# Kernel optimization log

Measured on AMD Instinct MI355X. Metric: run time of the kernel, lower is better.

Reference implementation:

```python
import jax, jax.numpy as jnp
import numpy as np
import math

D_MODEL = 1024
D_HIDDEN = 64
H = 16
B = 2
N = 2048


def softmax_one(x, axis=-1):
    # exp(x - max) / (1 + sum(exp(x - max))) -- matches the torch code exactly
    m = jnp.max(x, axis=axis, keepdims=True)
    e = jnp.exp(x - m)
    return e / (1.0 + jnp.sum(e, axis=axis, keepdims=True))


def setup_inputs() -> dict:
    key = jax.random.key(0)
    ks = jax.random.split(key, 8)
    queries = jax.random.normal(ks[0], (B, N, D_MODEL), dtype=jnp.float32)
    keys = jax.random.normal(ks[1], (B, N, D_MODEL), dtype=jnp.float32)
    values = jax.random.normal(ks[2], (B, N, D_MODEL), dtype=jnp.float32)
    std = 0.02
    Wq = std * jax.random.normal(ks[3], (H * D_HIDDEN, D_MODEL), dtype=jnp.float32)
    Wk = std * jax.random.normal(ks[4], (H * D_HIDDEN, D_MODEL), dtype=jnp.float32)
    Wv = std * jax.random.normal(ks[5], (H * D_HIDDEN, D_MODEL), dtype=jnp.float32)
    Wo = std * jax.random.normal(ks[6], (D_MODEL, H * D_HIDDEN), dtype=jnp.float32)
    bq = jnp.zeros((H * D_HIDDEN,), jnp.float32)
    bk = jnp.zeros((H * D_HIDDEN,), jnp.float32)
    bv = jnp.zeros((H * D_HIDDEN,), jnp.float32)
    bo = jnp.zeros((D_MODEL,), jnp.float32)
    return {"queries": queries, "keys": keys, "values": values,
            "Wq": Wq, "bq": bq, "Wk": Wk, "bk": bk,
            "Wv": Wv, "bv": bv, "Wo": Wo, "bo": bo}


def reference(queries, keys, values, Wq, bq, Wk, bk, Wv, bv, Wo, bo):
    b_s, nq, _ = queries.shape
    nk = keys.shape[1]
    # projections: (b, n, h*dh) -> (b, h, n, dh)
    q = (queries @ Wq.T + bq).reshape(b_s, nq, H, D_HIDDEN).transpose(0, 2, 1, 3)
    k = (keys @ Wk.T + bk).reshape(b_s, nk, H, D_HIDDEN).transpose(0, 2, 1, 3)
    v = (values @ Wv.T + bv).reshape(b_s, nk, H, D_HIDDEN).transpose(0, 2, 1, 3)
    scale = 1.0 / math.sqrt(D_HIDDEN)
    scores = jnp.einsum('bhqd,bhkd->bhqk', q, k) * scale  # (b, h, nq, nk)
    attn = softmax_one(scores, axis=-1)  # dropout disabled (eval)
    out = jnp.einsum('bhqk,bhkd->bhqd', attn, v)  # (b, h, nq, dh)
    out = out.transpose(0, 2, 1, 3).reshape(b_s, nq, H * D_HIDDEN)
    out = out @ Wo.T + bo
    present = jnp.stack((k, v))  # (2, b, h, nk, dh)
    return (out, present)
```

## Files before the change

kernel.cpp:

```cpp
#include <hip/hip_runtime.h>
#include <math.h>

#define D_MODEL 1024
#define DH 64
#define NH 16
#define BS 2
#define SEQ 2048
#define MTOT (BS*SEQ)

typedef _Float16 f16x8 __attribute__((ext_vector_type(8)));
typedef _Float16 f16x4 __attribute__((ext_vector_type(4)));
typedef float f32x4 __attribute__((ext_vector_type(4)));
typedef unsigned int u32;

__device__ __forceinline__ void load_lds16(const void* g, void* l) {
    __builtin_amdgcn_global_load_lds(
        (const __attribute__((address_space(1))) u32*)g,
        (__attribute__((address_space(3))) u32*)l, 16, 0, 0);
}

__global__ __launch_bounds__(256) void convert_all_kernel(
    const float* __restrict__ s0, const float* __restrict__ s1, const float* __restrict__ s2,
    const float* __restrict__ s3, const float* __restrict__ s4, const float* __restrict__ s5,
    const float* __restrict__ s6,
    _Float16* __restrict__ d0, _Float16* __restrict__ d1, _Float16* __restrict__ d2,
    _Float16* __restrict__ d3, _Float16* __restrict__ d4, _Float16* __restrict__ d5,
    _Float16* __restrict__ d6, int nX, int nW)
{
    int y = blockIdx.y;
    const float* s; _Float16* d; int n;
    switch (y) {
        case 0: s = s0; d = d0; n = nX; break;
        case 1: s = s1; d = d1; n = nX; break;
        case 2: s = s2; d = d2; n = nX; break;
        case 3: s = s3; d = d3; n = nW; break;
        case 4: s = s4; d = d4; n = nW; break;
        case 5: s = s5; d = d5; n = nW; break;
        default: s = s6; d = d6; n = nW; break;
    }
    int i = (blockIdx.x * 256 + threadIdx.x) * 8;
    if (i < n) {
        float4 a = *(const float4*)(s + i);
        float4 b = *(const float4*)(s + i + 4);
        f16x8 o;
        o[0] = (_Float16)a.x; o[1] = (_Float16)a.y; o[2] = (_Float16)a.z; o[3] = (_Float16)a.w;
        o[4] = (_Float16)b.x; o[5] = (_Float16)b.y; o[6] = (_Float16)b.z; o[7] = (_Float16)b.w;
        *(f16x8*)(d + i) = o;
    }
}

__global__ __launch_bounds__(256) void qkv_proj_kernel(
    const _Float16* __restrict__ Xq, const _Float16* __restrict__ Xk, const _Float16* __restrict__ Xv,
    const _Float16* __restrict__ Wq, const _Float16* __restrict__ Wk, const _Float16* __restrict__ Wv,
    const float* __restrict__ bq, const float* __restrict__ bk, const float* __restrict__ bv,
    _Float16* __restrict__ qh, _Float16* __restrict__ kh,
    float* __restrict__ outp)
{
    __shared__ __align__(16) _Float16 ldsA[128][64];
    __shared__ __align__(16) _Float16 ldsB[128][64];

    const int jb = blockIdx.x >> 5;
    const int ib = blockIdx.x & 31;
    const int id = jb >> 3;
    const int col0 = (jb & 7) << 7;
    const int row0 = ib << 7;

    const _Float16* X  = (id == 0) ? Xq : (id == 1) ? Xk : Xv;
    const _Float16* W  = (id == 0) ? Wq : (id == 1) ? Wk : Wv;
    const float* bias  = (id == 0) ? bq : (id == 1) ? bk : bv;

    const int tid = threadIdx.x;
    const int w = tid >> 6, lane = tid & 63;
    const int quad = lane >> 4, l16 = lane & 15;
    const int wm = (w >> 1) << 6, wn = (w & 1) << 6;

    const int r_loc = lane >> 3;
    const int sg = ((lane & 7) ^ r_loc) << 3;

    const f32x4 zero = {0.f, 0.f, 0.f, 0.f};
    f32x4 acc[4][4];
#pragma unroll
    for (int i = 0; i < 4; i++)
#pragma unroll
        for (int j = 0; j < 4; j++) acc[i][j] = zero;

    for (int k0 = 0; k0 < D_MODEL; k0 += 64) {
        __syncthreads();
#pragma unroll
        for (int i = 0; i < 4; i++) {
            int r = i * 32 + w * 8 + r_loc;
            load_lds16(X + (size_t)(row0 + r) * D_MODEL + k0 + sg, &ldsA[i * 32 + w * 8][0]);
            load_lds16(W + (size_t)(col0 + r) * D_MODEL + k0 + sg, &ldsB[i * 32 + w * 8][0]);
        }
        __syncthreads();
#pragma unroll
        for (int kk = 0; kk < 2; kk++) {
            f16x8 af[4], bfr[4];
#pragma unroll
            for (int mi = 0; mi < 4; mi++)
                af[mi]  = *(const f16x8*)&ldsA[wm + mi*16 + l16][(((kk<<2) + quad) ^ (l16 & 7)) << 3];
#pragma unroll
            for (int ni = 0; ni < 4; ni++)
                bfr[ni] = *(const f16x8*)&ldsB[wn + ni*16 + l16][(((kk<<2) + quad) ^ (l16 & 7)) << 3];
#pragma unroll
            for (int mi = 0; mi < 4; mi++)
#pragma unroll
                for (int ni = 0; ni < 4; ni++)
                    acc[mi][ni] = __builtin_amdgcn_mfma_f32_16x16x32_f16(af[mi], bfr[ni], acc[mi][ni], 0, 0, 0);
        }
    }

    const size_t OUT0 = (size_t)MTOT * D_MODEL;
    const size_t PRES = (size_t)BS * NH * SEQ * DH;
#pragma unroll
    for (int ni = 0; ni < 4; ni++) {
        int gn = col0 + wn + ni * 16 + l16;
        float bias_v = bias[gn];
        int h = gn >> 6, d = gn & 63;
#pragma unroll
        for (int mi = 0; mi < 4; mi++) {
#pragma unroll
            for (int r = 0; r < 4; r++) {
                int gm = row0 + wm + mi * 16 + quad * 4 + r;
                float val = acc[mi][ni][r] + bias_v;
                int b = gm >> 11, n = gm & 2047;
                size_t bh = (size_t)(b * NH + h);
                size_t idx = (bh * SEQ + n) * DH + d;
                if (id == 0) {
                    qh[idx] = (_Float16)val;
                } else if (id == 1) {
                    outp[OUT0 + idx] = val;
                    kh[idx] = (_Float16)val;
                } else {
                    outp[OUT0 + PRES + idx] = val;
                }
            }
        }
    }
}

__global__ __launch_bounds__(256) void vtrans_kernel(
    const float* __restrict__ p1, _Float16* __restrict__ vt)
{
    const int bh = blockIdx.x >> 6, nt = blockIdx.x & 63;
    const int tid = threadIdx.x;
    const int d = tid & 63, n8 = tid >> 6;
    const int n0 = nt * 32 + n8 * 8;
    const float* src = p1 + ((size_t)bh * SEQ + n0) * DH + d;
    f16x8 o;
#pragma unroll
    for (int i = 0; i < 8; i++) o[i] = (_Float16)src[(size_t)i * DH];
    *(f16x8*)(vt + ((size_t)bh * DH + d) * SEQ + n0) = o;
}

__global__ __launch_bounds__(512) void attn_kernel(
    const _Float16* __restrict__ qh, const _Float16* __restrict__ kh,
    const _Float16* __restrict__ vt, _Float16* __restrict__ aout)
{
    __shared__ __align__(16) _Float16 Kt[2][64][76];
    __shared__ __align__(16) _Float16 Vt[2][64][76];

    const int bh = blockIdx.x & 31;
    const int qt = blockIdx.x >> 5;
    const int b = bh >> 4, h = bh & 15;
    const int tid = threadIdx.x;
    const int w = tid >> 6, lane = tid & 63;
    const int quad = lane >> 4, l16 = lane & 15;
    const int qr0 = qt * 128 + w * 16;

    const _Float16* Qb = qh + (size_t)bh * SEQ * DH;
    const _Float16* Kb = kh + (size_t)bh * SEQ * DH;
    const _Float16* Vb = vt + (size_t)bh * DH * SEQ;

    const float QSCALE = 0.125f * 1.44269504f;
    f16x8 aq[2];
#pragma unroll
    for (int ks = 0; ks < 2; ks++) {
        f16x8 t = *(const f16x8*)(Qb + (size_t)(qr0 + l16) * DH + ks * 32 + quad * 8);
#pragma unroll
        for (int j = 0; j < 8; j++) t[j] = (_Float16)((float)t[j] * QSCALE);
        aq[ks] = t;
    }

    const int sr = tid >> 3, sc = (tid & 7) << 3;

    *(f16x8*)&Kt[0][sr][sc] = *(const f16x8*)(Kb + (size_t)sr * DH + sc);
    *(f16x8*)&Vt[0][sr][sc] = *(const f16x8*)(Vb + (size_t)sr * SEQ + sc);
    __syncthreads();

    float m2 = -INFINITY, lsum = 0.f;
    const f32x4 zero = {0.f, 0.f, 0.f, 0.f};
    f32x4 accO[4];
#pragma unroll
    for (int db = 0; db < 4; db++) accO[db] = zero;

    for (int t = 0; t < SEQ / 64; t++) {
        const int cur = t & 1;
        const int kc = t * 64;

        f16x8 kr, vr;
        if (t + 1 < SEQ / 64) {
            kr = *(const f16x8*)(Kb + (size_t)(kc + 64 + sr) * DH + sc);
            vr = *(const f16x8*)(Vb + (size_t)sr * SEQ + kc + 64 + sc);
        }

        f32x4 sT[4];
#pragma unroll
        for (int nb = 0; nb < 4; nb++) sT[nb] = zero;
#pragma unroll
        for (int ks = 0; ks < 2; ks++)
#pragma unroll
            for (int nb = 0; nb < 4; nb++) {
                f16x8 kf = *(const f16x8*)&Kt[cur][nb*16 + l16][ks*32 + quad*8];
                sT[nb] = __builtin_amdgcn_mfma_f32_16x16x32_f16(kf, aq[ks], sT[nb], 0, 0, 0);
            }

        f16x4 pf[4];
#pragma unroll
        for (int nb = 0; nb < 4; nb++)
#pragma unroll
            for (int r = 0; r < 4; r++) {
                float s = sT[nb][r];
                m2 = fmaxf(m2, s);
                float e = __builtin_amdgcn_exp2f(s);
                lsum += e;
                pf[nb][r] = (_Float16)e;
            }

#pragma unroll
        for (int db = 0; db < 4; db++)
#pragma unroll
            for (int nb = 0; nb < 4; nb++) {
                f16x4 vf = *(const f16x4*)&Vt[cur][db*16 + l16][nb*16 + quad*4];
                accO[db] = __builtin_amdgcn_mfma_f32_16x16x16f16(vf, pf[nb], accO[db], 0, 0, 0);
            }

        if (t + 1 < SEQ / 64) {
            *(f16x8*)&Kt[cur ^ 1][sr][sc] = kr;
            *(f16x8*)&Vt[cur ^ 1][sr][sc] = vr;
        }
        __syncthreads();
    }

    m2 = fmaxf(m2, __shfl_xor(m2, 16));
    m2 = fmaxf(m2, __shfl_xor(m2, 32));
    lsum += __shfl_xor(lsum, 16);
    lsum += __shfl_xor(lsum, 32);

    const float inv = 1.f / (__builtin_amdgcn_exp2f(m2) + lsum);
    const int q = qr0 + l16;
    _Float16* orow = aout + ((size_t)b * SEQ + q) * D_MODEL + h * DH + quad * 4;
#pragma unroll
    for (int db = 0; db < 4; db++) {
        f16x4 o;
#pragma unroll
        for (int r = 0; r < 4; r++) o[r] = (_Float16)(accO[db][r] * inv);
        *(f16x4*)(orow + db * 16) = o;
    }
}

__global__ __launch_bounds__(256) void out_proj_kernel(
    const _Float16* __restrict__ aout, const _Float16* __restrict__ Wo,
    const float* __restrict__ bo, float* __restrict__ outp)
{
    __shared__ __align__(16) _Float16 ldsA[64][64];
    __shared__ __align__(16) _Float16 ldsB[128][64];

    const int jb = blockIdx.x >> 6;
    const int ib = blockIdx.x & 63;
    const int col0 = jb << 7, row0 = ib << 6;
    const int tid = threadIdx.x;
    const int w = tid >> 6, lane = tid & 63;
    const int quad = lane >> 4, l16 = lane & 15;
    const int wm = (w >> 1) << 5, wn = (w & 1) << 6;

    const int r_loc = lane >> 3;
    const int sg = ((lane & 7) ^ r_loc) << 3;

    const f32x4 zero = {0.f, 0.f, 0.f, 0.f};
    f32x4 acc[2][4];
#pragma unroll
    for (int i = 0; i < 2; i++)
#pragma unroll
        for (int j = 0; j < 4; j++) acc[i][j] = zero;

    for (int k0 = 0; k0 < D_MODEL; k0 += 64) {
        __syncthreads();
#pragma unroll
        for (int i = 0; i < 2; i++) {
            int r = i * 32 + w * 8 + r_loc;
            load_lds16(aout + (size_t)(row0 + r) * D_MODEL + k0 + sg, &ldsA[i * 32 + w * 8][0]);
        }
#pragma unroll
        for (int i = 0; i < 4; i++) {
            int r = i * 32 + w * 8 + r_loc;
            load_lds16(Wo + (size_t)(col0 + r) * D_MODEL + k0 + sg, &ldsB[i * 32 + w * 8][0]);
        }
        __syncthreads();
#pragma unroll
        for (int kk = 0; kk < 2; kk++) {
            f16x8 af[2], bfr[4];
#pragma unroll
            for (int mi = 0; mi < 2; mi++)
                af[mi]  = *(const f16x8*)&ldsA[wm + mi*16 + l16][(((kk<<2) + quad) ^ (l16 & 7)) << 3];
#pragma unroll
            for (int ni = 0; ni < 4; ni++)
                bfr[ni] = *(const f16x8*)&ldsB[wn + ni*16 + l16][(((kk<<2) + quad) ^ (l16 & 7)) << 3];
#pragma unroll
            for (int mi = 0; mi < 2; mi++)
#pragma unroll
                for (int ni = 0; ni < 4; ni++)
                    acc[mi][ni] = __builtin_amdgcn_mfma_f32_16x16x32_f16(af[mi], bfr[ni], acc[mi][ni], 0, 0, 0);
        }
    }

#pragma unroll
    for (int ni = 0; ni < 4; ni++) {
        int gn = col0 + wn + ni * 16 + l16;
        float bias_v = bo[gn];
#pragma unroll
        for (int mi = 0; mi < 2; mi++)
#pragma unroll
            for (int r = 0; r < 4; r++) {
                int gm = row0 + wm + mi * 16 + quad * 4 + r;
                outp[(size_t)gm * D_MODEL + gn] = acc[mi][ni][r] + bias_v;
            }
    }
}

extern "C" void kernel_launch(void* const* d_in, const int* in_sizes, int n_in,
                              void* d_out, int out_size, void* d_ws, size_t ws_size,
                              hipStream_t stream)
{
    const float* queries = (const float*)d_in[0];
    const float* keys    = (const float*)d_in[1];
    const float* values  = (const float*)d_in[2];
    const float* Wq = (const float*)d_in[3];
    const float* bq = (const float*)d_in[4];
    const float* Wk = (const float*)d_in[5];
    const float* bk = (const float*)d_in[6];
    const float* Wv = (const float*)d_in[7];
    const float* bv = (const float*)d_in[8];
    const float* Wo = (const float*)d_in[9];
    const float* bo = (const float*)d_in[10];
    float* outp = (float*)d_out;

    const size_t NELT = (size_t)BS * NH * SEQ * DH;
    const size_t XN   = (size_t)MTOT * D_MODEL;
    const size_t WN   = (size_t)D_MODEL * D_MODEL;
    _Float16* qh   = (_Float16*)d_ws;
    _Float16* kh   = qh + NELT;
    _Float16* vt   = kh + NELT;
    _Float16* aout = vt + NELT;
    _Float16* Xfq  = aout + NELT;
    _Float16* Xfk  = Xfq + XN;
    _Float16* Xfv  = Xfk + XN;
    _Float16* Wfq  = Xfv + XN;
    _Float16* Wfk  = Wfq + WN;
    _Float16* Wfv  = Wfk + WN;
    _Float16* Wfo  = Wfv + WN;

    const size_t OUT0 = (size_t)MTOT * D_MODEL;
    const size_t PRES = NELT;
    const float* present1 = outp + OUT0 + PRES;

    convert_all_kernel<<<dim3((int)(XN/2048), 7), dim3(256), 0, stream>>>(
        queries, keys, values, Wq, Wk, Wv, Wo,
        Xfq, Xfk, Xfv, Wfq, Wfk, Wfv, Wfo, (int)XN, (int)WN);

    qkv_proj_kernel<<<dim3(768), dim3(256), 0, stream>>>(
        Xfq, Xfk, Xfv, Wfq, Wfk, Wfv, bq, bk, bv, qh, kh, outp);
    vtrans_kernel<<<dim3(2048), dim3(256), 0, stream>>>(present1, vt);
    attn_kernel<<<dim3(512), dim3(512), 0, stream>>>(qh, kh, vt, aout);
    out_proj_kernel<<<dim3(512), dim3(256), 0, stream>>>(aout, Wfo, bo, outp);
}
```

Measured before the change: 242.6 us.

## Double-buffer LDS tiles in QKV and output projection GEMMs

Both projection GEMM kernels now use two LDS buffers per operand. The next k-tile is prefetched with global_load_lds while MFMAs run on the current tile, with one barrier per iteration instead of two. This aims to hide global load latency behind compute, at the cost of doubled LDS use (64KB in the QKV kernel), which may lower occupancy.

```diff
diff --git a/kernel.cpp b/kernel.cpp
--- a/kernel.cpp
+++ b/kernel.cpp
@@ -56,8 +56,8 @@
     _Float16* __restrict__ qh, _Float16* __restrict__ kh,
     float* __restrict__ outp)
 {
-    __shared__ __align__(16) _Float16 ldsA[128][64];
-    __shared__ __align__(16) _Float16 ldsB[128][64];
+    __shared__ __align__(16) _Float16 ldsA[2][128][64];
+    __shared__ __align__(16) _Float16 ldsB[2][128][64];
 
     const int jb = blockIdx.x >> 5;
     const int ib = blockIdx.x & 31;
@@ -84,30 +84,44 @@
 #pragma unroll
         for (int j = 0; j < 4; j++) acc[i][j] = zero;
 
-    for (int k0 = 0; k0 < D_MODEL; k0 += 64) {
-        __syncthreads();
-#pragma unroll
-        for (int i = 0; i < 4; i++) {
-            int r = i * 32 + w * 8 + r_loc;
-            load_lds16(X + (size_t)(row0 + r) * D_MODEL + k0 + sg, &ldsA[i * 32 + w * 8][0]);
-            load_lds16(W + (size_t)(col0 + r) * D_MODEL + k0 + sg, &ldsB[i * 32 + w * 8][0]);
-        }
-        __syncthreads();
+#pragma unroll
+    for (int i = 0; i < 4; i++) {
+        int r = i * 32 + w * 8;
+        load_lds16(X + (size_t)(row0 + r + r_loc) * D_MODEL + sg, &ldsA[0][r][0]);
+        load_lds16(W + (size_t)(col0 + r + r_loc) * D_MODEL + sg, &ldsB[0][r][0]);
+    }
+    __syncthreads();
+
+    for (int t = 0; t < D_MODEL / 64; t++) {
+        const int cur = t & 1;
+
+        if (t + 1 < D_MODEL / 64) {
+            const int k1 = (t + 1) << 6;
+#pragma unroll
+            for (int i = 0; i < 4; i++) {
+                int r = i * 32 + w * 8;
+                load_lds16(X + (size_t)(row0 + r + r_loc) * D_MODEL + k1 + sg, &ldsA[cur ^ 1][r][0]);
+                load_lds16(W + (size_t)(col0 + r + r_loc) * D_MODEL + k1 + sg, &ldsB[cur ^ 1][r][0]);
+            }
+        }
+
 #pragma unroll
         for (int kk = 0; kk < 2; kk++) {
             f16x8 af[4], bfr[4];
 #pragma unroll
             for (int mi = 0; mi < 4; mi++)
-                af[mi]  = *(const f16x8*)&ldsA[wm + mi*16 + l16][(((kk<<2) + quad) ^ (l16 & 7)) << 3];
+                af[mi]  = *(const f16x8*)&ldsA[cur][wm + mi*16 + l16][(((kk<<2) + quad) ^ (l16 & 7)) << 3];
 #pragma unroll
             for (int ni = 0; ni < 4; ni++)
-                bfr[ni] = *(const f16x8*)&ldsB[wn + ni*16 + l16][(((kk<<2) + quad) ^ (l16 & 7)) << 3];
+                bfr[ni] = *(const f16x8*)&ldsB[cur][wn + ni*16 + l16][(((kk<<2) + quad) ^ (l16 & 7)) << 3];
 #pragma unroll
             for (int mi = 0; mi < 4; mi++)
 #pragma unroll
                 for (int ni = 0; ni < 4; ni++)
                     acc[mi][ni] = __builtin_amdgcn_mfma_f32_16x16x32_f16(af[mi], bfr[ni], acc[mi][ni], 0, 0, 0);
         }
+
+        __syncthreads();
     }
 
     const size_t OUT0 = (size_t)MTOT * D_MODEL;
@@ -263,8 +277,8 @@
     const _Float16* __restrict__ aout, const _Float16* __restrict__ Wo,
     const float* __restrict__ bo, float* __restrict__ outp)
 {
-    __shared__ __align__(16) _Float16 ldsA[64][64];
-    __shared__ __align__(16) _Float16 ldsB[128][64];
+    __shared__ __align__(16) _Float16 ldsA[2][64][64];
+    __shared__ __align__(16) _Float16 ldsB[2][128][64];
 
     const int jb = blockIdx.x >> 6;
     const int ib = blockIdx.x & 63;
@@ -284,34 +298,52 @@
 #pragma unroll
         for (int j = 0; j < 4; j++) acc[i][j] = zero;
 
-    for (int k0 = 0; k0 < D_MODEL; k0 += 64) {
-        __syncthreads();
-#pragma unroll
-        for (int i = 0; i < 2; i++) {
-            int r = i * 32 + w * 8 + r_loc;
-            load_lds16(aout + (size_t)(row0 + r) * D_MODEL + k0 + sg, &ldsA[i * 32 + w * 8][0]);
-        }
-#pragma unroll
-        for (int i = 0; i < 4; i++) {
-            int r = i * 32 + w * 8 + r_loc;
-            load_lds16(Wo + (size_t)(col0 + r) * D_MODEL + k0 + sg, &ldsB[i * 32 + w * 8][0]);
-        }
-        __syncthreads();
+#pragma unroll
+    for (int i = 0; i < 2; i++) {
+        int r = i * 32 + w * 8;
+        load_lds16(aout + (size_t)(row0 + r + r_loc) * D_MODEL + sg, &ldsA[0][r][0]);
+    }
+#pragma unroll
+    for (int i = 0; i < 4; i++) {
+        int r = i * 32 + w * 8;
+        load_lds16(Wo + (size_t)(col0 + r + r_loc) * D_MODEL + sg, &ldsB[0][r][0]);
+    }
+    __syncthreads();
+
+    for (int t = 0; t < D_MODEL / 64; t++) {
+        const int cur = t & 1;
+
+        if (t + 1 < D_MODEL / 64) {
+            const int k1 = (t + 1) << 6;
+#pragma unroll
+            for (int i = 0; i < 2; i++) {
+                int r = i * 32 + w * 8;
+                load_lds16(aout + (size_t)(row0 + r + r_loc) * D_MODEL + k1 + sg, &ldsA[cur ^ 1][r][0]);
+            }
+#pragma unroll
+            for (int i = 0; i < 4; i++) {
+                int r = i * 32 + w * 8;
+                load_lds16(Wo + (size_t)(col0 + r + r_loc) * D_MODEL + k1 + sg, &ldsB[cur ^ 1][r][0]);
+            }
+        }
+
 #pragma unroll
         for (int kk = 0; kk < 2; kk++) {
             f16x8 af[2], bfr[4];
 #pragma unroll
             for (int mi = 0; mi < 2; mi++)
-                af[mi]  = *(const f16x8*)&ldsA[wm + mi*16 + l16][(((kk<<2) + quad) ^ (l16 & 7)) << 3];
+                af[mi]  = *(const f16x8*)&ldsA[cur][wm + mi*16 + l16][(((kk<<2) + quad) ^ (l16 & 7)) << 3];
 #pragma unroll
             for (int ni = 0; ni < 4; ni++)
-                bfr[ni] = *(const f16x8*)&ldsB[wn + ni*16 + l16][(((kk<<2) + quad) ^ (l16 & 7)) << 3];
+                bfr[ni] = *(const f16x8*)&ldsB[cur][wn + ni*16 + l16][(((kk<<2) + quad) ^ (l16 & 7)) << 3];
 #pragma unroll
             for (int mi = 0; mi < 2; mi++)
 #pragma unroll
                 for (int ni = 0; ni < 4; ni++)
                     acc[mi][ni] = __builtin_amdgcn_mfma_f32_16x16x32_f16(af[mi], bfr[ni], acc[mi][ni], 0, 0, 0);
         }
+
+        __syncthreads();
     }
 
 #pragma unroll
```

Measured after the change: 245.7 us. About the same (+1.3%).
